# Kernel tuning notes

Hardware: AMD Instinct MI355X
Metric: run time of the kernel (lower is better)

The kernel has to match this reference:

```python
import jax, jax.numpy as jnp
import numpy as np

N = 100000          # instances in the bag
L_IN = 784          # 28*28
C = 128             # size[1]
H = 2               # n_heads = len(temperature)
S = C // H          # step = 64
D = S // 2          # per-head hidden dim ('small') = 32
TEMP = jnp.array([1.0, 1.0], dtype=jnp.float32)  # temperature per head


def setup_inputs() -> dict:
    key = jax.random.key(0)
    ks = jax.random.split(key, 8)
    h = jax.random.normal(ks[0], (N, L_IN), dtype=jnp.float32)
    # shared FC: Linear(784, 128) (xavier-normal-ish init, zero bias)
    W0 = jax.random.normal(ks[1], (L_IN, C), dtype=jnp.float32) * (2.0 / (L_IN + C)) ** 0.5
    b0 = jnp.zeros((C,), dtype=jnp.float32)
    # per-head gated attention nets, stacked over head axis
    Wa = jax.random.normal(ks[2], (H, S, D), dtype=jnp.float32) * (2.0 / (S + D)) ** 0.5
    ba = jnp.zeros((H, D), dtype=jnp.float32)
    Wb = jax.random.normal(ks[3], (H, S, D), dtype=jnp.float32) * (2.0 / (S + D)) ** 0.5
    bb = jnp.zeros((H, D), dtype=jnp.float32)
    Wc = jax.random.normal(ks[4], (H, D, 1), dtype=jnp.float32) * (2.0 / (D + 1)) ** 0.5
    bc = jnp.zeros((H, 1), dtype=jnp.float32)
    # bag-level classifier: Linear(128, 1)
    Wcls = jax.random.normal(ks[5], (C, 1), dtype=jnp.float32) * (2.0 / (C + 1)) ** 0.5
    bcls = jnp.zeros((1,), dtype=jnp.float32)
    return {"h": h, "W0": W0, "b0": b0, "Wa": Wa, "ba": ba,
            "Wb": Wb, "bb": bb, "Wc": Wc, "bc": bc,
            "Wcls": Wcls, "bcls": bcls}


def reference(h, W0, b0, Wa, ba, Wb, bb, Wc, bc, Wcls, bcls):
    # shared FC + ReLU: [N,784] -> [N,128]
    x = jax.nn.relu(h @ W0 + b0)
    x = x.reshape(-1, H, S)                                  # [N,H,S]
    # gated attention per head, batched over heads via einsum
    a = jnp.tanh(jnp.einsum('nhs,hsd->nhd', x, Wa) + ba)     # [N,H,D]
    g = jax.nn.sigmoid(jnp.einsum('nhs,hsd->nhd', x, Wb) + bb)
    A = (jnp.einsum('nhd,hdo->nho', a * g, Wc) + bc)[..., 0] # [N,H]
    A = A / TEMP                                             # temperature scaling per head
    Aw = jax.nn.softmax(A, axis=0)                           # softmax over instances N
    # weighted instance pooling: [1, H*S] = [1, 128]
    M = jnp.einsum('nh,nhs->hs', Aw, x).reshape(1, H * S)
    logits = (M @ Wcls + bcls)[:, 0]                         # [1]
    Y_prob = jax.nn.sigmoid(logits)
    Y_hat = (Y_prob >= 0.5).astype(jnp.float32)
    return (Y_prob, Y_hat)
```

## Files before the change

### kernel.cpp

```cpp
#include <hip/hip_runtime.h>
#include <stdint.h>
#include <math.h>

typedef unsigned short u16;
typedef unsigned int   u32;
typedef __bf16 bf16x8 __attribute__((ext_vector_type(8)));
typedef float  f32x4  __attribute__((ext_vector_type(4)));

#define L_IN 784
#define KT2 25

__device__ __forceinline__ u32 f2bf(float f){
    u32 u = __float_as_uint(f);
    return (u + 0x7fffu + ((u >> 16) & 1u)) >> 16;
}

__device__ __forceinline__ void gload16(const void* g, void* l){
    __builtin_amdgcn_global_load_lds(
        (const __attribute__((address_space(1))) unsigned char*)g,
        (__attribute__((address_space(3))) unsigned char*)l, 16, 0, 0);
}

__global__ void prep_all(const float* __restrict__ W0, const float* __restrict__ Wa,
                         const float* __restrict__ Wb, u16* __restrict__ Bimg,
                         u16* __restrict__ Wab){
    int idx = blockIdx.x * 256 + threadIdx.x;
    if (idx < KT2 * 32 * 128){
        int col = idx & 127, k = idx >> 7;
        float v = (k < L_IN) ? W0[idx] : 0.f;
        int kt2 = k >> 5, lk = (k >> 3) & 3, j = k & 7;
        Bimg[((kt2 * 8 + (col >> 4)) << 9) + (lk * 16 + (col & 15)) * 8 + j]
            = (u16)f2bf(v);
    } else if (idx < KT2 * 32 * 128 + 16384){
        int i2 = idx - KT2 * 32 * 128;
        int jj = i2 & 7, l = (i2 >> 3) & 63, ks = (i2 >> 9) & 1;
        int nt = (i2 >> 10) & 1, h = (i2 >> 11) & 1, mat = (i2 >> 12) & 1;
        int s = ks * 32 + (l >> 4) * 8 + jj, d = nt * 16 + (l & 15);
        const float* W = mat ? Wb : Wa;
        Wab[i2] = (u16)f2bf(W[h * 2048 + s * 32 + d]);
    }
}

__global__ __launch_bounds__(256, 3)
void fc_fused(const float* __restrict__ hG, const u16* __restrict__ Bimg,
              const u16* __restrict__ Wab, const float* __restrict__ b0,
              const float* __restrict__ ba, const float* __restrict__ bb,
              const float* __restrict__ Wc, const float* __restrict__ bc,
              float* __restrict__ partials, int N){
    __shared__ __align__(16) char Asm[3 * 16384];

    const int t    = threadIdx.x;
    const int lane = t & 63;
    const int w    = t >> 6;
    const int lr   = lane & 15;
    const int lk   = lane >> 4;
    const int gb   = blockIdx.x;
    const long rowBase = (long)gb * 128;

    const int cs = (t & 7) ^ ((t >> 3) & 7);
    const float* srcp[4];
    #pragma unroll
    for (int j = 0; j < 4; ++j){
        long grow = rowBase + j * 32 + (t >> 3);
        if (grow >= N) grow = N - 1;
        srcp[j] = hG + grow * L_IN + cs * 4;
    }

    f32x4 acc[2][8];
    #pragma unroll
    for (int mt = 0; mt < 2; ++mt)
        #pragma unroll
        for (int nt = 0; nt < 8; ++nt) acc[mt][nt] = (f32x4)0.f;

    auto stage = [&](int kt, char* buf){
        const int off = (kt == KT2 - 1 && cs >= 4) ? 0 : kt * 32;
        #pragma unroll
        for (int j = 0; j < 4; ++j)
            gload16(srcp[j] + off, buf + (j * 256 + t) * 16);
    };

    char* p0 = &Asm[0];
    char* p1 = &Asm[16384];
    char* p2 = &Asm[32768];
    stage(0, p0);
    stage(1, p1);

    #pragma unroll 1
    for (int kt = 0; kt < KT2; ++kt){
        if (kt == 0) __syncthreads();
        else         __builtin_amdgcn_s_barrier();
        __builtin_amdgcn_sched_barrier(0);

        const u16* bp = Bimg + (size_t)kt * 4096 + lane * 8;
        bf16x8 bfr[8];
        #pragma unroll
        for (int nt = 0; nt < 8; ++nt)
            bfr[nt] = *(const bf16x8*)(bp + nt * 512);
        __builtin_amdgcn_sched_barrier(0);

        if (kt + 2 < KT2) stage(kt + 2, p2);
        __builtin_amdgcn_sched_barrier(0);

        #pragma unroll
        for (int mt = 0; mt < 2; ++mt){
            const int rA = w * 32 + mt * 16 + lr;
            const char* base = p0 + rA * 128;
            f32x4 lo = *(const f32x4*)(base + (((lk * 2)    ) ^ (rA & 7)) * 16);
            f32x4 hi = *(const f32x4*)(base + (((lk * 2) + 1) ^ (rA & 7)) * 16);
            bf16x8 af;
            #pragma unroll
            for (int j = 0; j < 4; ++j){
                af[j]     = (__bf16)lo[j];
                af[4 + j] = (__bf16)hi[j];
            }
            #pragma unroll
            for (int nt = 0; nt < 8; ++nt)
                acc[mt][nt] = __builtin_amdgcn_mfma_f32_16x16x32_bf16(
                                  af, bfr[nt], acc[mt][nt], 0, 0, 0);
        }
        char* tmp = p0; p0 = p1; p1 = p2; p2 = tmp;
    }

    __syncthreads();

    u16*   xs   = (u16*)&Asm[0];
    float* pbuf = (float*)&Asm[32768];
    #pragma unroll
    for (int mt = 0; mt < 2; ++mt)
        #pragma unroll
        for (int nt = 0; nt < 8; ++nt){
            float bias = b0[nt * 16 + lr];
            #pragma unroll
            for (int j = 0; j < 4; ++j){
                float v = acc[mt][nt][j] + bias;
                v = v > 0.f ? v : 0.f;
                acc[mt][nt][j] = v;
                int row = w * 32 + mt * 16 + lk * 4 + j;
                int col = nt * 16 + lr;
                xs[row * 128 + (((col >> 3) ^ (row & 15)) << 3) + (col & 7)] = (u16)f2bf(v);
            }
        }
    __syncthreads();

    float eh[2][2][4];
    #pragma unroll
    for (int mt = 0; mt < 2; ++mt)
        #pragma unroll
        for (int h = 0; h < 2; ++h){
            const int row = w * 32 + mt * 16 + lr;
            bf16x8 xa[2];
            #pragma unroll
            for (int ks = 0; ks < 2; ++ks){
                int ch = (h * 8 + ks * 4 + lk) ^ (row & 15);
                xa[ks] = *(const bf16x8*)&xs[row * 128 + ch * 8];
            }
            f32x4 Ca[2], Cg[2];
            #pragma unroll
            for (int nt = 0; nt < 2; ++nt){ Ca[nt] = (f32x4)0.f; Cg[nt] = (f32x4)0.f; }
            #pragma unroll
            for (int nt = 0; nt < 2; ++nt)
                #pragma unroll
                for (int ks = 0; ks < 2; ++ks){
                    bf16x8 wfa = *(const bf16x8*)(Wab + ((size_t)(h*4 + nt*2 + ks) << 9) + lane * 8);
                    bf16x8 wfb = *(const bf16x8*)(Wab + ((size_t)(8 + h*4 + nt*2 + ks) << 9) + lane * 8);
                    Ca[nt] = __builtin_amdgcn_mfma_f32_16x16x32_bf16(xa[ks], wfa, Ca[nt], 0, 0, 0);
                    Cg[nt] = __builtin_amdgcn_mfma_f32_16x16x32_bf16(xa[ks], wfb, Cg[nt], 0, 0, 0);
                }
            float pj[4];
            #pragma unroll
            for (int j = 0; j < 4; ++j){
                float s = 0.f;
                #pragma unroll
                for (int nt = 0; nt < 2; ++nt){
                    int d = h * 32 + nt * 16 + lr;
                    float av = tanhf(Ca[nt][j] + ba[d]);
                    float gv = 1.f / (1.f + expf(-(Cg[nt][j] + bb[d])));
                    s += av * gv * Wc[d];
                }
                pj[j] = s;
            }
            #pragma unroll
            for (int m = 1; m <= 8; m <<= 1)
                #pragma unroll
                for (int j = 0; j < 4; ++j)
                    pj[j] += __shfl_xor(pj[j], m, 64);
            #pragma unroll
            for (int j = 0; j < 4; ++j){
                long grow = rowBase + w * 32 + mt * 16 + lk * 4 + j;
                eh[mt][h][j] = (grow < (long)N) ? expf(pj[j] + bc[h]) : 0.f;
            }
        }

    float p[8];
    #pragma unroll
    for (int nt = 0; nt < 8; ++nt){
        const int h = nt >> 2;
        float s = 0.f;
        #pragma unroll
        for (int mt = 0; mt < 2; ++mt)
            #pragma unroll
            for (int j = 0; j < 4; ++j) s += eh[mt][h][j] * acc[mt][nt][j];
        p[nt] = s;
    }
    #pragma unroll
    for (int m = 16; m <= 32; m <<= 1)
        #pragma unroll
        for (int nt = 0; nt < 8; ++nt)
            p[nt] += __shfl_xor(p[nt], m, 64);
    float es0 = 0.f, es1 = 0.f;
    #pragma unroll
    for (int mt = 0; mt < 2; ++mt)
        #pragma unroll
        for (int j = 0; j < 4; ++j){ es0 += eh[mt][0][j]; es1 += eh[mt][1][j]; }
    es0 += __shfl_xor(es0, 16, 64); es0 += __shfl_xor(es0, 32, 64);
    es1 += __shfl_xor(es1, 16, 64); es1 += __shfl_xor(es1, 32, 64);

    if (lk == 0){
        #pragma unroll
        for (int nt = 0; nt < 8; ++nt)
            pbuf[w * 132 + nt * 16 + lr] = p[nt];
    }
    if (lane == 0){
        pbuf[w * 132 + 128] = es0;
        pbuf[w * 132 + 129] = es1;
    }
    __syncthreads();
    if (t < 130){
        float s = pbuf[t] + pbuf[132 + t] + pbuf[264 + t] + pbuf[396 + t];
        partials[(size_t)gb * 132 + t] = s;
    }
}

__global__ __launch_bounds__(256)
void reduce1(const float* __restrict__ partials, float* __restrict__ red, int nb){
    const int b = blockIdx.x, t = threadIdx.x;
    if (t >= 130) return;
    float a0 = 0.f, a1 = 0.f;
    for (int r = b; r < nb; r += 256){
        a0 += partials[(size_t)r * 132 + t];
        if (r + 128 < nb) a1 += partials[(size_t)(r + 128) * 132 + t];
    }
    red[b * 132 + t] = a0 + a1;
}

__global__ __launch_bounds__(256)
void finalize2(const float* __restrict__ red, const float* __restrict__ Wcls,
               const float* __restrict__ bcls, float* __restrict__ out){
    __shared__ double colD[2][130];
    __shared__ float  M_s[128];
    const int t = threadIdx.x;
    const int c = t & 127, rh = t >> 7;
    {
        double s = 0.0;
        for (int r = rh * 64; r < rh * 64 + 64; r += 4){
            s += (double)red[(r + 0) * 132 + c] + (double)red[(r + 1) * 132 + c]
               + (double)red[(r + 2) * 132 + c] + (double)red[(r + 3) * 132 + c];
        }
        colD[rh][c] = s;
    }
    if (t < 4){
        int cc = 128 + (t & 1), hh = t >> 1;
        double s = 0.0;
        for (int r = hh * 64; r < hh * 64 + 64; r += 4){
            s += (double)red[(r + 0) * 132 + cc] + (double)red[(r + 1) * 132 + cc]
               + (double)red[(r + 2) * 132 + cc] + (double)red[(r + 3) * 132 + cc];
        }
        colD[hh][cc] = s;
    }
    __syncthreads();
    if (t < 128)
        M_s[t] = (float)((colD[0][t] + colD[1][t]) /
                         (colD[0][128 + (t >> 6)] + colD[1][128 + (t >> 6)]));
    __syncthreads();
    if (t < 64){
        double d = (double)M_s[t] * (double)Wcls[t]
                 + (double)M_s[t + 64] * (double)Wcls[t + 64];
        #pragma unroll
        for (int m = 1; m < 64; m <<= 1) d += __shfl_xor(d, m, 64);
        if (t == 0){
            double lg = d + (double)bcls[0];
            out[0] = (float)(1.0 / (1.0 + exp(-lg)));
            out[1] = (lg >= 0.0) ? 1.f : 0.f;
        }
    }
}

extern "C" void kernel_launch(void* const* d_in, const int* in_sizes, int n_in,
                              void* d_out, int out_size, void* d_ws, size_t ws_size,
                              hipStream_t stream){
    const float* hG   = (const float*)d_in[0];
    const float* W0   = (const float*)d_in[1];
    const float* b0   = (const float*)d_in[2];
    const float* Wa   = (const float*)d_in[3];
    const float* ba   = (const float*)d_in[4];
    const float* Wb   = (const float*)d_in[5];
    const float* bb   = (const float*)d_in[6];
    const float* Wc   = (const float*)d_in[7];
    const float* bc   = (const float*)d_in[8];
    const float* Wcls = (const float*)d_in[9];
    const float* bcls = (const float*)d_in[10];

    const int N     = in_sizes[0] / L_IN;
    const int nb128 = (N + 127) / 128;

    char* ws = (char*)d_ws;
    u16* Bimg = (u16*)ws;
    u16* Wab  = (u16*)(ws + 262144);
    size_t poff = 262144 + 16384;
    float* partials = (float*)(ws + poff);
    size_t roff = poff + (((size_t)nb128 * 132 * 4 + 4095) & ~(size_t)4095);
    float* red  = (float*)(ws + roff);

    prep_all <<<(KT2 * 32 * 128 + 16384 + 255) / 256, 256, 0, stream>>>(W0, Wa, Wb, Bimg, Wab);
    fc_fused <<<nb128, 256, 0, stream>>>(hG, Bimg, Wab, b0, ba, bb, Wc, bc,
                                         partials, N);
    reduce1  <<<128, 256, 0, stream>>>(partials, red, nb128);
    finalize2<<<1, 256, 0, stream>>>(red, Wcls, bcls, (float*)d_out);
}
```

Baseline: 124.7 us.

## Stage W0 bf16 tiles through LDS with double buffering and explicit waitcnt

The B operand (bf16 W0 image) is now staged into LDS with async global_load_lds into a double buffer, instead of each wave loading it straight from global memory every k-step. The barrier moves to the end of each iteration, with an explicit vmcnt wait so the next A and B tiles are resident before the barrier. LDS use grows to 64KB, so launch bounds drop from 3 to 2 blocks per CU. This trades occupancy for fewer redundant global/L2 reads of B across the four waves.

```diff
diff --git a/kernel.cpp b/kernel.cpp
--- a/kernel.cpp
+++ b/kernel.cpp
@@ -28,8 +28,8 @@
     if (idx < KT2 * 32 * 128){
         int col = idx & 127, k = idx >> 7;
         float v = (k < L_IN) ? W0[idx] : 0.f;
-        int kt2 = k >> 5, lk = (k >> 3) & 3, j = k & 7;
-        Bimg[((kt2 * 8 + (col >> 4)) << 9) + (lk * 16 + (col & 15)) * 8 + j]
+        int kt = k >> 5, lk = (k >> 3) & 3, j = k & 7;
+        Bimg[((kt * 8 + (col >> 4)) << 9) + (lk * 16 + (col & 15)) * 8 + j]
             = (u16)f2bf(v);
     } else if (idx < KT2 * 32 * 128 + 16384){
         int i2 = idx - KT2 * 32 * 128;
@@ -41,13 +41,13 @@
     }
 }
 
-__global__ __launch_bounds__(256, 3)
+__global__ __launch_bounds__(256, 2)
 void fc_fused(const float* __restrict__ hG, const u16* __restrict__ Bimg,
               const u16* __restrict__ Wab, const float* __restrict__ b0,
               const float* __restrict__ ba, const float* __restrict__ bb,
               const float* __restrict__ Wc, const float* __restrict__ bc,
               float* __restrict__ partials, int N){
-    __shared__ __align__(16) char Asm[3 * 16384];
+    __shared__ __align__(16) char Asm[4 * 16384];
 
     const int t    = threadIdx.x;
     const int lane = t & 63;
@@ -65,6 +65,7 @@
         if (grow >= N) grow = N - 1;
         srcp[j] = hG + grow * L_IN + cs * 4;
     }
+    const char* BimgB = (const char*)Bimg;
 
     f32x4 acc[2][8];
     #pragma unroll
@@ -72,39 +73,43 @@
         #pragma unroll
         for (int nt = 0; nt < 8; ++nt) acc[mt][nt] = (f32x4)0.f;
 
-    auto stage = [&](int kt, char* buf){
+    auto stageA = [&](int kt, char* buf){
         const int off = (kt == KT2 - 1 && cs >= 4) ? 0 : kt * 32;
         #pragma unroll
         for (int j = 0; j < 4; ++j)
             gload16(srcp[j] + off, buf + (j * 256 + t) * 16);
     };
-
-    char* p0 = &Asm[0];
-    char* p1 = &Asm[16384];
-    char* p2 = &Asm[32768];
-    stage(0, p0);
-    stage(1, p1);
+    auto stageB = [&](int kt, char* buf){
+        #pragma unroll
+        for (int i = 0; i < 2; ++i)
+            gload16(BimgB + (size_t)kt * 8192 + i * 4096 + t * 16,
+                    buf + i * 4096 + t * 16);
+    };
+
+    char* pa0 = &Asm[0];     char* pa1 = &Asm[16384]; char* pa2 = &Asm[32768];
+    char* pbR = &Asm[49152]; char* pbW = &Asm[57344];
+
+    stageA(0, pa0);
+    stageA(1, pa1);
+    stageB(0, pbR);
+    __syncthreads();
 
     #pragma unroll 1
     for (int kt = 0; kt < KT2; ++kt){
-        if (kt == 0) __syncthreads();
-        else         __builtin_amdgcn_s_barrier();
         __builtin_amdgcn_sched_barrier(0);
-
-        const u16* bp = Bimg + (size_t)kt * 4096 + lane * 8;
+        if (kt + 1 < KT2) stageB(kt + 1, pbW);
+        if (kt + 2 < KT2) stageA(kt + 2, pa2);
+        __builtin_amdgcn_sched_barrier(0);
+
         bf16x8 bfr[8];
         #pragma unroll
         for (int nt = 0; nt < 8; ++nt)
-            bfr[nt] = *(const bf16x8*)(bp + nt * 512);
-        __builtin_amdgcn_sched_barrier(0);
-
-        if (kt + 2 < KT2) stage(kt + 2, p2);
-        __builtin_amdgcn_sched_barrier(0);
+            bfr[nt] = *(const bf16x8*)(pbR + nt * 1024 + lane * 16);
 
         #pragma unroll
         for (int mt = 0; mt < 2; ++mt){
             const int rA = w * 32 + mt * 16 + lr;
-            const char* base = p0 + rA * 128;
+            const char* base = pa0 + rA * 128;
             f32x4 lo = *(const f32x4*)(base + (((lk * 2)    ) ^ (rA & 7)) * 16);
             f32x4 hi = *(const f32x4*)(base + (((lk * 2) + 1) ^ (rA & 7)) * 16);
             bf16x8 af;
@@ -118,7 +123,16 @@
                 acc[mt][nt] = __builtin_amdgcn_mfma_f32_16x16x32_bf16(
                                   af, bfr[nt], acc[mt][nt], 0, 0, 0);
         }
-        char* tmp = p0; p0 = p1; p1 = p2; p2 = tmp;
+
+        if (kt + 1 < KT2){
+            if (kt + 2 < KT2) asm volatile("s_waitcnt vmcnt(4)" ::: "memory");
+            else              asm volatile("s_waitcnt vmcnt(0)" ::: "memory");
+            __builtin_amdgcn_sched_barrier(0);
+            __builtin_amdgcn_s_barrier();
+            __builtin_amdgcn_sched_barrier(0);
+        }
+        char* ta = pa0; pa0 = pa1; pa1 = pa2; pa2 = ta;
+        char* tb = pbR; pbR = pbW; pbW = tb;
     }
 
     __syncthreads();
```

Result: faster. 105.8 us (-15.1%).
